# Optimization experiments

Hardware: AMD Instinct MI355X
Metric: run time of the kernel (lower is better)

Reference implementation:

```python
import jax, jax.numpy as jnp
import numpy as np

B = 256      # graphs per batch
N = 512      # nodes per graph
FEAT = 64    # num_features
H = 64       # nhid
DEG = 16     # avg degree
RATIO = 0.5  # pooling_ratio
E = B * N * DEG


def setup_inputs() -> dict:
    key = jax.random.key(0)
    ks = jax.random.split(key, 12)
    # edges constructed within each graph via offsets
    src_loc = jax.random.randint(ks[0], (B, N * DEG), 0, N)
    dst_loc = jax.random.randint(ks[1], (B, N * DEG), 0, N)
    offs = (jnp.arange(B) * N)[:, None]
    edge_src = (src_loc + offs).reshape(-1).astype(jnp.int32)
    edge_dst = (dst_loc + offs).reshape(-1).astype(jnp.int32)
    batch = jnp.repeat(jnp.arange(B, dtype=jnp.int32), N)
    x = jax.random.normal(ks[2], (B * N, FEAT), dtype=jnp.float32)
    edge_attr = jax.random.uniform(ks[3], (E,), dtype=jnp.float32) + 0.1
    s1 = 1.0 / np.sqrt(FEAT)
    s2 = 1.0 / np.sqrt(H)
    return {
        "x": x,
        "edge_attr": edge_attr,
        "W1": jax.random.normal(ks[4], (FEAT, H), jnp.float32) * s1,
        "b1": jnp.zeros((H,), jnp.float32),
        "Wp1": jax.random.normal(ks[5], (H, 1), jnp.float32) * s2,
        "bp1": jnp.zeros((1,), jnp.float32),
        "W2": jax.random.normal(ks[6], (H, H), jnp.float32) * s2,
        "b2": jnp.zeros((H,), jnp.float32),
        "Wp2": jax.random.normal(ks[7], (H, 1), jnp.float32) * s2,
        "bp2": jnp.zeros((1,), jnp.float32),
        "edge_src": edge_src,
        "edge_dst": edge_dst,
        "batch": batch,
    }


def gcn_conv(x, W, b, src, dst, ew, n):
    """PyG GCNConv: sym-normalized weighted adjacency + self-loops (weight 1)."""
    h = x @ W                                   # [n, out]
    deg = jnp.zeros((n,), x.dtype).at[dst].add(ew) + 1.0  # self-loop adds 1
    dinv = jax.lax.rsqrt(deg)
    coef = dinv[dst] * ew * dinv[src]           # [E]
    out = jnp.zeros_like(h).at[dst].add(coef[:, None] * h[src])
    out = out + h * (1.0 / deg)[:, None]        # self-loop term: deg^-0.5 * 1 * deg^-0.5
    return out + b


def sag_pool(x, src, dst, ew, Wp, bp, n_per):
    """SAGPool: score = GCNConv(x)->1, per-graph top-k, gate by tanh(score),
    filter edges (dropped edges represented by zero weight)."""
    n = x.shape[0]
    score = gcn_conv(x, Wp, bp, src, dst, ew, n)[:, 0]   # [n]
    k = int(np.ceil(RATIO * n_per))
    _, idx = jax.lax.top_k(score.reshape(B, n_per), k)   # [B, k] local indices
    perm = (idx + (jnp.arange(B) * n_per)[:, None]).reshape(-1)
    xn = x[perm] * jnp.tanh(score[perm])[:, None]        # [B*k, H]
    newid = jnp.full((n,), -1, jnp.int32).at[perm].set(
        jnp.arange(B * k, dtype=jnp.int32))
    ns, nd = newid[src], newid[dst]
    valid = (ns >= 0) & (nd >= 0)
    ew2 = jnp.where(valid, ew, 0.0)
    ns = jnp.where(valid, ns, 0)
    nd = jnp.where(valid, nd, 0)
    return xn, ns, nd, ew2, k


def readout(x, k):
    """[gmp || gap] per graph; each graph has exactly k nodes, contiguous."""
    xg = x.reshape(B, k, -1)
    return jnp.concatenate([xg.max(axis=1), xg.mean(axis=1)], axis=1)  # [B, 2H]


def reference(x, edge_attr, W1, b1, Wp1, bp1, W2, b2, Wp2, bp2,
              edge_src, edge_dst, batch):
    n0 = x.shape[0]
    h = jax.nn.relu(gcn_conv(x, W1, b1, edge_src, edge_dst, edge_attr, n0))
    h, s1, d1, w1e, k1 = sag_pool(h, edge_src, edge_dst, edge_attr, Wp1, bp1, N)
    x1 = readout(h, k1)
    h = jax.nn.relu(gcn_conv(h, W2, b2, s1, d1, w1e, B * k1))
    h, _, _, _, k2 = sag_pool(h, s1, d1, w1e, Wp2, bp2, k1)
    x2 = readout(h, k2)
    return (x1 + x2) / 2.0
```

## Files before the change

### kernel.cpp

```cpp
#include <hip/hip_runtime.h>
#include <math.h>

#define BG   256
#define NN   512
#define EPG  (NN * 16)
#define NE   (BG * EPG)
#define N0   (BG * NN)
#define K1   256
#define N1_  (BG * K1)
#define K2   128

__device__ __forceinline__ float4 f4fma(float s, float4 a, float4 c) {
    c.x = fmaf(s, a.x, c.x); c.y = fmaf(s, a.y, c.y);
    c.z = fmaf(s, a.z, c.z); c.w = fmaf(s, a.w, c.w);
    return c;
}

__device__ __forceinline__ void gemm_tile(const float* __restrict__ shx,
                                          const float4* __restrict__ W4,
                                          int row0, int rg, int cg, float4 a[4]) {
    float4 acc0 = make_float4(0.f, 0.f, 0.f, 0.f);
    float4 acc1 = acc0, acc2 = acc0, acc3 = acc0;
#pragma unroll
    for (int k4 = 0; k4 < 16; ++k4) {
        float4 xv0 = *(const float4*)&shx[(row0 + rg * 4 + 0) * 68 + k4 * 4];
        float4 xv1 = *(const float4*)&shx[(row0 + rg * 4 + 1) * 68 + k4 * 4];
        float4 xv2 = *(const float4*)&shx[(row0 + rg * 4 + 2) * 68 + k4 * 4];
        float4 xv3 = *(const float4*)&shx[(row0 + rg * 4 + 3) * 68 + k4 * 4];
        float4 wv0 = W4[(k4 * 4 + 0) * 16 + cg];
        float4 wv1 = W4[(k4 * 4 + 1) * 16 + cg];
        float4 wv2 = W4[(k4 * 4 + 2) * 16 + cg];
        float4 wv3 = W4[(k4 * 4 + 3) * 16 + cg];
        acc0 = f4fma(xv0.x, wv0, acc0); acc0 = f4fma(xv0.y, wv1, acc0);
        acc0 = f4fma(xv0.z, wv2, acc0); acc0 = f4fma(xv0.w, wv3, acc0);
        acc1 = f4fma(xv1.x, wv0, acc1); acc1 = f4fma(xv1.y, wv1, acc1);
        acc1 = f4fma(xv1.z, wv2, acc1); acc1 = f4fma(xv1.w, wv3, acc1);
        acc2 = f4fma(xv2.x, wv0, acc2); acc2 = f4fma(xv2.y, wv1, acc2);
        acc2 = f4fma(xv2.z, wv2, acc2); acc2 = f4fma(xv2.w, wv3, acc2);
        acc3 = f4fma(xv3.x, wv0, acc3); acc3 = f4fma(xv3.y, wv1, acc3);
        acc3 = f4fma(xv3.z, wv2, acc3); acc3 = f4fma(xv3.w, wv3, acc3);
    }
    a[0] = acc0; a[1] = acc1; a[2] = acc2; a[3] = acc3;
}

template <int NPG, int K, bool REMAP, bool FINAL>
__global__ __launch_bounds__(1024)
void stage_kernel(const int* __restrict__ esrc, const int* __restrict__ edst,
                  const float* __restrict__ eatt, const int* __restrict__ nid_in,
                  int* __restrict__ nid_out, int2* __restrict__ pairs,
                  const float4* __restrict__ X4, const float4* __restrict__ W4,
                  const float4* __restrict__ b4, const float4* __restrict__ wp4,
                  const float* __restrict__ bp,
                  float4* __restrict__ xn4, float* __restrict__ xr,
                  const float* __restrict__ x1r, float* __restrict__ out) {
    constexpr int PASSES = NPG / 32;
    constexpr int LPN = 1024 / NPG;
    constexpr int LOG_LPN = (LPN == 2) ? 1 : 2;
    constexpr int QF = 16 / LPN;
    constexpr int RLOG = (NPG == 512) ? 9 : 8;
    constexpr int RCH = NPG * NPG / 1024;
    constexpr int SH_A = NPG * 68;
    constexpr int TILES = NPG / 64, TPP = TILES / 2, TB = TPP / 2 ? TPP / 2 : 1;
    __shared__ __align__(16) float smem[SH_A + 4096 + 2 * NPG];
    float* shx = smem;
    float* S   = smem + SH_A;
    int*   cnt   = (int*)S;
    int*   rstl  = (int*)S + NPG;
    float* sdinv = S + 2 * NPG;
    int*   perm  = (int*)S + 3 * NPG;
    float* shp   = S + 4 * NPG;
    int*   scn   = (int*)S + 4 * NPG;
    float* wsum  = S + 5 * NPG;
    float* sbw   = S + 6 * NPG;
    int*   hist  = (int*)S + 6 * NPG + 64;
    int*   wtot  = (int*)S + 6 * NPG + 128;
    float4* smx  = (float4*)S;
    float4* ssm  = (float4*)(S + 2048);
    float* ssc   = S + 4096;
    int*   rnk   = (int*)S + 4096 + NPG;

    int g = blockIdx.x, nbase = g * NPG, e0 = g * EPG;
    int t = threadIdx.x;
    int lane16 = t & 15, lane = t & 63;

    int ed[16], es[16]; float ea[16];
    int xs = 0, xval = 0;
    float4 accA[TB][4], accB[TB][4];
    int tl = t - 512, q2 = (t & 511) >> 8, tq = t & 255;
    int rgg = tq >> 4, cgg = tq & 15;

    if (t < 512) {
        for (int i = t; i < NPG; i += 512) { cnt[i] = 0; wsum[i] = 0.f; }
        const int4*   edst4 = (const int4*)(edst + e0);
        const int4*   esrc4 = (const int4*)(esrc + e0);
        const float4* eatt4 = (const float4*)(eatt + e0);
#pragma unroll
        for (int c = 0; c < 4; ++c) {
            int ch = t + c * 512;
            int4   dd = edst4[ch];
            int4   ss = esrc4[ch];
            float4 ww = eatt4[ch];
            ed[c * 4 + 0] = dd.x; ed[c * 4 + 1] = dd.y; ed[c * 4 + 2] = dd.z; ed[c * 4 + 3] = dd.w;
            es[c * 4 + 0] = ss.x; es[c * 4 + 1] = ss.y; es[c * 4 + 2] = ss.z; es[c * 4 + 3] = ss.w;
            ea[c * 4 + 0] = ww.x; ea[c * 4 + 1] = ww.y; ea[c * 4 + 2] = ww.z; ea[c * 4 + 3] = ww.w;
        }
        if (REMAP) {
#pragma unroll
            for (int j = 0; j < 16; ++j) { ed[j] = nid_in[ed[j]]; es[j] = nid_in[es[j]]; }
        }
    } else {
        for (int i = tl; i < NPG * 16; i += 512) {
            int r = i >> 4, c4 = i & 15;
            *(float4*)&shx[r * 68 + c4 * 4] = X4[(size_t)nbase * 16 + i];
        }
        if (tl < 64) { sbw[tl] = ((const float*)b4)[tl]; hist[tl] = 0; }
        for (int i = tl; i < NPG; i += 512) rnk[i] = 0;
    }
    __syncthreads();
    if (t < 512) {
#pragma unroll
        for (int j = 0; j < 16; ++j) {
            bool valid = !REMAP || (ed[j] >= 0 && es[j] >= 0);
            if (valid) {
                int dl = ed[j] - nbase;
                atomicAdd(&cnt[dl], 1);
                atomicAdd(&wsum[dl], ea[j]);
            }
        }
    } else {
#pragma unroll
        for (int b = 0; b < TB; ++b)
            gemm_tile(shx, W4, (q2 * TPP + b) * 64, rgg, cgg, accA[b]);
    }
    __syncthreads();
    if (t < 512) {
        int wvid = t >> 6;
        xval = (t < NPG) ? cnt[t] : 0;
        xs = xval;
#pragma unroll
        for (int off = 1; off < 64; off <<= 1) {
            int v = __shfl_up(xs, off, 64);
            if (lane >= off) xs += v;
        }
        if (lane == 63) wtot[wvid] = xs;
    } else {
#pragma unroll
        for (int b = 0; b < TB; ++b) {
            int row0 = (q2 * TPP + b) * 64;
            *(float4*)&shx[(row0 + rgg * 4 + 0) * 68 + cgg * 4] = accA[b][0];
            *(float4*)&shx[(row0 + rgg * 4 + 1) * 68 + cgg * 4] = accA[b][1];
            *(float4*)&shx[(row0 + rgg * 4 + 2) * 68 + cgg * 4] = accA[b][2];
            *(float4*)&shx[(row0 + rgg * 4 + 3) * 68 + cgg * 4] = accA[b][3];
        }
    }
    __syncthreads();
    if (t < 512) {
        int wvid = t >> 6;
        int woff = 0;
#pragma unroll
        for (int w = 0; w < 8; ++w) { int wt = wtot[w]; if (w < wvid) woff += wt; }
        xs += woff;
        if (t < NPG) {
            int st = xs - xval;
            rstl[t] = st;
            sdinv[t] = rsqrtf(wsum[t] + 1.0f);
            scn[t] = st;
        }
    } else {
#pragma unroll
        for (int b = 0; b < TB; ++b)
            gemm_tile(shx, W4, (q2 * TPP + TB + b) * 64, rgg, cgg, accB[b]);
    }
    __syncthreads();
    if (t < 512) {
#pragma unroll
        for (int j = 0; j < 16; ++j) {
            bool valid = !REMAP || (ed[j] >= 0 && es[j] >= 0);
            if (valid) {
                int dl = ed[j] - nbase, sl = es[j] - nbase;
                float cf = sdinv[dl] * ea[j] * sdinv[sl];
                int slot = atomicAdd(&scn[dl], 1);
                pairs[e0 + slot] = make_int2(sl, __float_as_int(cf));
            }
        }
    } else {
#pragma unroll
        for (int b = 0; b < TB; ++b) {
            int row0 = (q2 * TPP + TB + b) * 64;
            *(float4*)&shx[(row0 + rgg * 4 + 0) * 68 + cgg * 4] = accB[b][0];
            *(float4*)&shx[(row0 + rgg * 4 + 1) * 68 + cgg * 4] = accB[b][1];
            *(float4*)&shx[(row0 + rgg * 4 + 2) * 68 + cgg * 4] = accB[b][2];
            *(float4*)&shx[(row0 + rgg * 4 + 3) * 68 + cgg * 4] = accB[b][3];
        }
    }
    __syncthreads();

    for (int i = t; i < NPG; i += 1024) {
        int c = min(cnt[i], 63);
        atomicAdd(&hist[c], 1);
    }
    __syncthreads();
    if (t < 64) {
        int v = hist[t], s = v;
#pragma unroll
        for (int off = 1; off < 64; off <<= 1) {
            int u = __shfl_up(s, off, 64);
            if (lane >= off) s += u;
        }
        hist[t] = s - v;
    }
    __syncthreads();
    for (int i = t; i < NPG; i += 1024) {
        int c = min(cnt[i], 63);
        int pos = atomicAdd(&hist[c], 1);
        perm[pos] = i;
    }
    __syncthreads();
    {
        int idx2 = t >> LOG_LPN;
        int half = t & (LPN - 1);
        int nl = perm[idx2];
        int st = rstl[nl], cn = cnt[nl];
        float di = sdinv[nl], dii = di * di;
        const int2* pb = pairs + e0 + st;
        int fb = half * QF;
        float4 acc[QF];
#pragma unroll
        for (int c = 0; c < QF; ++c) {
            float4 xv = *(const float4*)&shx[nl * 68 + (fb + c) * 4];
            acc[c].x = fmaf(xv.x, dii, sbw[(fb + c) * 4 + 0]);
            acc[c].y = fmaf(xv.y, dii, sbw[(fb + c) * 4 + 1]);
            acc[c].z = fmaf(xv.z, dii, sbw[(fb + c) * 4 + 2]);
            acc[c].w = fmaf(xv.w, dii, sbw[(fb + c) * 4 + 3]);
        }
        int2 p0 = (cn > 0) ? pb[0] : make_int2(0, 0);
        int2 p1 = (cn > 1) ? pb[1] : make_int2(0, 0);
        for (int j = 0; j < cn; ++j) {
            int2 p2 = (j + 2 < cn) ? pb[j + 2] : make_int2(0, 0);
            float cfv = __int_as_float(p0.y);
            int   s   = p0.x;
#pragma unroll
            for (int c = 0; c < QF; ++c)
                acc[c] = f4fma(cfv, *(const float4*)&shx[s * 68 + (fb + c) * 4], acc[c]);
            p0 = p1; p1 = p2;
        }
#pragma unroll
        for (int c = 0; c < QF; ++c) {
            acc[c].x = fmaxf(acc[c].x, 0.f); acc[c].y = fmaxf(acc[c].y, 0.f);
            acc[c].z = fmaxf(acc[c].z, 0.f); acc[c].w = fmaxf(acc[c].w, 0.f);
        }
        __syncthreads();
#pragma unroll
        for (int c = 0; c < QF; ++c)
            *(float4*)&shx[nl * 68 + (fb + c) * 4] = acc[c];
    }
    __syncthreads();
    if (t < 512) {
        int wv8 = t >> 6, sub4 = (t >> 4) & 3;
        float4 w4 = wp4[lane16];
#pragma unroll
        for (int p = 0; p < PASSES; ++p) {
            int n2 = p * 32 + wv8 * 4 + sub4;
            float4 a = *(const float4*)&shx[n2 * 68 + lane16 * 4];
            float tt = a.x * w4.x + a.y * w4.y + a.z * w4.z + a.w * w4.w;
            tt += __shfl_xor(tt, 1, 64); tt += __shfl_xor(tt, 2, 64);
            tt += __shfl_xor(tt, 4, 64); tt += __shfl_xor(tt, 8, 64);
            if (lane16 == 0) shp[n2] = tt;
        }
    }
    __syncthreads();
    if (t < NPG) {
        int i = perm[t];
        int st = rstl[i], cn = cnt[i];
        float di = sdinv[i];
        const int2* pb = pairs + e0 + st;
        float a = fmaf(shp[i], di * di, bp[0]);
        int2 q0 = (cn > 0) ? pb[0] : make_int2(0, 0);
        int2 q1 = (cn > 1) ? pb[1] : make_int2(0, 0);
        for (int j = 0; j < cn; ++j) {
            int2 q2v = (j + 2 < cn) ? pb[j + 2] : make_int2(0, 0);
            a = fmaf(__int_as_float(q0.y), shp[q0.x], a);
            q0 = q1; q1 = q2v;
        }
        ssc[i] = a;
    }
    __syncthreads();
    {
        int part = t >> RLOG;
        int i = t & (NPG - 1);
        float si = ssc[i];
        int j0 = part * RCH;
        int rank = 0;
        for (int j = j0; j < j0 + RCH; j += 4) {
            float4 sj = *(const float4*)&ssc[j];
            rank += (sj.x > si) || (sj.x == si && j     < i);
            rank += (sj.y > si) || (sj.y == si && j + 1 < i);
            rank += (sj.z > si) || (sj.z == si && j + 2 < i);
            rank += (sj.w > si) || (sj.w == si && j + 3 < i);
        }
        atomicAdd(&rnk[i], rank);
    }
    __syncthreads();
    if (!FINAL)
        for (int i = t; i < NPG; i += 1024)
            nid_out[nbase + i] = (rnk[i] < K) ? (g * K + rnk[i]) : -1;
    float4 mx = make_float4(-3.402823466e38f, -3.402823466e38f, -3.402823466e38f, -3.402823466e38f);
    float4 sm = make_float4(0.f, 0.f, 0.f, 0.f);
    if (t < 512) {
        int wv8 = t >> 6, sub4 = (t >> 4) & 3;
#pragma unroll
        for (int p = 0; p < PASSES; ++p) {
            int n2 = p * 32 + wv8 * 4 + sub4;
            int r = rnk[n2];
            if (r < K) {
                float gt = tanhf(ssc[n2]);
                float4 v = *(const float4*)&shx[n2 * 68 + lane16 * 4];
                v.x *= gt; v.y *= gt; v.z *= gt; v.w *= gt;
                if (!FINAL) xn4[((size_t)g * K + r) * 16 + lane16] = v;
                mx.x = fmaxf(mx.x, v.x); mx.y = fmaxf(mx.y, v.y);
                mx.z = fmaxf(mx.z, v.z); mx.w = fmaxf(mx.w, v.w);
                sm.x += v.x; sm.y += v.y; sm.z += v.z; sm.w += v.w;
            }
        }
    }
    int grp = t >> 4;
    __syncthreads();
    if (t < 512) {
        smx[grp * 16 + lane16] = mx;
        ssm[grp * 16 + lane16] = sm;
    }
    __syncthreads();
    if (grp == 0) {
#pragma unroll
        for (int u = 1; u < 32; ++u) {
            float4 a = smx[u * 16 + lane16], b = ssm[u * 16 + lane16];
            mx.x = fmaxf(mx.x, a.x); mx.y = fmaxf(mx.y, a.y);
            mx.z = fmaxf(mx.z, a.z); mx.w = fmaxf(mx.w, a.w);
            sm.x += b.x; sm.y += b.y; sm.z += b.z; sm.w += b.w;
        }
        float invK = 1.f / K;
        int c = lane16 * 4;
        float mr[4] = {mx.x, mx.y, mx.z, mx.w};
        float ar[4] = {sm.x * invK, sm.y * invK, sm.z * invK, sm.w * invK};
#pragma unroll
        for (int u = 0; u < 4; ++u) {
            if (FINAL) {
                out[g * 128 + c + u]      = 0.5f * (x1r[g * 128 + c + u]      + mr[u]);
                out[g * 128 + 64 + c + u] = 0.5f * (x1r[g * 128 + 64 + c + u] + ar[u]);
            } else {
                xr[g * 128 + c + u]      = mr[u];
                xr[g * 128 + 64 + c + u] = ar[u];
            }
        }
    }
}

extern "C" void kernel_launch(void* const* d_in, const int* in_sizes, int n_in,
                              void* d_out, int out_size, void* d_ws, size_t ws_size,
                              hipStream_t stream) {
    const float* x    = (const float*)d_in[0];
    const float* eatt = (const float*)d_in[1];
    const float* W1   = (const float*)d_in[2];
    const float* b1   = (const float*)d_in[3];
    const float* Wp1  = (const float*)d_in[4];
    const float* bp1  = (const float*)d_in[5];
    const float* W2   = (const float*)d_in[6];
    const float* b2   = (const float*)d_in[7];
    const float* Wp2  = (const float*)d_in[8];
    const float* bp2  = (const float*)d_in[9];
    const int*   esrc = (const int*)d_in[10];
    const int*   edst = (const int*)d_in[11];
    float* out = (float*)d_out;

    float* ws = (float*)d_ws;
    size_t o = 0;
    float* A    = ws + o; o += (size_t)N0 * 64;
    float* xn1  = ws + o; o += (size_t)N1_ * 64;
    int2*  prs  = (int2*)(ws + o); o += (size_t)NE * 2;
    int*   rst  = (int*)(ws + o); o += N0;
    int*   rcn  = (int*)(ws + o); o += N0;
    float* dinv = ws + o; o += N0;
    int*   nid  = (int*)(ws + o); o += N0;
    float* x1r  = ws + o; o += BG * 128;
    (void)A; (void)rst; (void)rcn; (void)dinv;

    stage_kernel<NN, K1, false, false><<<BG, 1024, 0, stream>>>(
        esrc, edst, eatt, nullptr, nid, prs,
        (const float4*)x, (const float4*)W1, (const float4*)b1,
        (const float4*)Wp1, bp1, (float4*)xn1, x1r, nullptr, nullptr);
    stage_kernel<K1, K2, true, true><<<BG, 1024, 0, stream>>>(
        esrc, edst, eatt, nid, nullptr, prs,
        (const float4*)xn1, (const float4*)W2, (const float4*)b2,
        (const float4*)Wp2, bp2, nullptr, nullptr, x1r, out);
}
```

Measured before the change: 257.3 us.

## Fuse both GCN+SAGPool stages into one per-graph kernel kept in shared memory

Merges the two stage launches into one kernel per graph. The pooled features, the node remap and the first-readout vector now stay in shared memory instead of round-tripping through global memory. CSR pair writes are staged through LDS in two halves so the global stores are coalesced, and all 1024 threads now do edge preprocessing instead of splitting work with the GEMM. The cost is that the GEMM no longer overlaps the edge phase, and there are more barriers and larger shared-memory use per block.

```diff
diff --git a/kernel.cpp b/kernel.cpp
--- a/kernel.cpp
+++ b/kernel.cpp
@@ -5,10 +5,6 @@
 #define NN   512
 #define EPG  (NN * 16)
 #define NE   (BG * EPG)
-#define N0   (BG * NN)
-#define K1   256
-#define N1_  (BG * K1)
-#define K2   128
 
 __device__ __forceinline__ float4 f4fma(float s, float4 a, float4 c) {
     c.x = fmaf(s, a.x, c.x); c.y = fmaf(s, a.y, c.y);
@@ -43,162 +39,128 @@
     a[0] = acc0; a[1] = acc1; a[2] = acc2; a[3] = acc3;
 }
 
-template <int NPG, int K, bool REMAP, bool FINAL>
 __global__ __launch_bounds__(1024)
-void stage_kernel(const int* __restrict__ esrc, const int* __restrict__ edst,
-                  const float* __restrict__ eatt, const int* __restrict__ nid_in,
-                  int* __restrict__ nid_out, int2* __restrict__ pairs,
-                  const float4* __restrict__ X4, const float4* __restrict__ W4,
-                  const float4* __restrict__ b4, const float4* __restrict__ wp4,
-                  const float* __restrict__ bp,
-                  float4* __restrict__ xn4, float* __restrict__ xr,
-                  const float* __restrict__ x1r, float* __restrict__ out) {
-    constexpr int PASSES = NPG / 32;
-    constexpr int LPN = 1024 / NPG;
-    constexpr int LOG_LPN = (LPN == 2) ? 1 : 2;
-    constexpr int QF = 16 / LPN;
-    constexpr int RLOG = (NPG == 512) ? 9 : 8;
-    constexpr int RCH = NPG * NPG / 1024;
-    constexpr int SH_A = NPG * 68;
-    constexpr int TILES = NPG / 64, TPP = TILES / 2, TB = TPP / 2 ? TPP / 2 : 1;
-    __shared__ __align__(16) float smem[SH_A + 4096 + 2 * NPG];
-    float* shx = smem;
-    float* S   = smem + SH_A;
+void mega_kernel(const int* __restrict__ esrc, const int* __restrict__ edst,
+                 const float* __restrict__ eatt, int2* __restrict__ pairs,
+                 const float4* __restrict__ X4,
+                 const float4* __restrict__ W1_4, const float4* __restrict__ b1_4,
+                 const float4* __restrict__ wp1_4, const float* __restrict__ bp1,
+                 const float4* __restrict__ W2_4, const float4* __restrict__ b2_4,
+                 const float4* __restrict__ wp2_4, const float* __restrict__ bp2,
+                 float* __restrict__ out) {
+    __shared__ __align__(16) float smem[40720];
+    float* shx  = smem;
+    float* S    = smem + 34816;
     int*   cnt   = (int*)S;
-    int*   rstl  = (int*)S + NPG;
-    float* sdinv = S + 2 * NPG;
-    int*   perm  = (int*)S + 3 * NPG;
-    float* shp   = S + 4 * NPG;
-    int*   scn   = (int*)S + 4 * NPG;
-    float* wsum  = S + 5 * NPG;
-    float* sbw   = S + 6 * NPG;
-    int*   hist  = (int*)S + 6 * NPG + 64;
-    int*   wtot  = (int*)S + 6 * NPG + 128;
-    float4* smx  = (float4*)S;
-    float4* ssm  = (float4*)(S + 2048);
-    float* ssc   = S + 4096;
-    int*   rnk   = (int*)S + 4096 + NPG;
-
-    int g = blockIdx.x, nbase = g * NPG, e0 = g * EPG;
+    int*   rstl  = (int*)S + 512;
+    float* sdinv = S + 1024;
+    int*   perm  = (int*)S + 1536;
+    int*   scn   = (int*)S + 2048;
+    float* shp   = S + 2048;
+    float* wsum  = S + 2560;
+    float* ssc   = S + 2560;
+    int*   rnk   = (int*)S + 3072;
+    float* sbw   = S + 3584;
+    int*   hist  = (int*)S + 3648;
+    int*   wtot  = (int*)S + 3712;
+    float* x1rs  = S + 3728;
+    float4* redx = (float4*)(S + 3856);
+
+    int g = blockIdx.x, nb1 = g * NN, e0 = g * EPG;
     int t = threadIdx.x;
     int lane16 = t & 15, lane = t & 63;
 
-    int ed[16], es[16]; float ea[16];
-    int xs = 0, xval = 0;
-    float4 accA[TB][4], accB[TB][4];
-    int tl = t - 512, q2 = (t & 511) >> 8, tq = t & 255;
-    int rgg = tq >> 4, cgg = tq & 15;
-
-    if (t < 512) {
-        for (int i = t; i < NPG; i += 512) { cnt[i] = 0; wsum[i] = 0.f; }
+    for (int i = t; i < NN; i += 1024) { cnt[i] = 0; wsum[i] = 0.f; }
+    __syncthreads();
+    {
         const int4*   edst4 = (const int4*)(edst + e0);
         const int4*   esrc4 = (const int4*)(esrc + e0);
         const float4* eatt4 = (const float4*)(eatt + e0);
-#pragma unroll
-        for (int c = 0; c < 4; ++c) {
-            int ch = t + c * 512;
-            int4   dd = edst4[ch];
-            int4   ss = esrc4[ch];
-            float4 ww = eatt4[ch];
-            ed[c * 4 + 0] = dd.x; ed[c * 4 + 1] = dd.y; ed[c * 4 + 2] = dd.z; ed[c * 4 + 3] = dd.w;
-            es[c * 4 + 0] = ss.x; es[c * 4 + 1] = ss.y; es[c * 4 + 2] = ss.z; es[c * 4 + 3] = ss.w;
-            ea[c * 4 + 0] = ww.x; ea[c * 4 + 1] = ww.y; ea[c * 4 + 2] = ww.z; ea[c * 4 + 3] = ww.w;
-        }
-        if (REMAP) {
-#pragma unroll
-            for (int j = 0; j < 16; ++j) { ed[j] = nid_in[ed[j]]; es[j] = nid_in[es[j]]; }
-        }
-    } else {
-        for (int i = tl; i < NPG * 16; i += 512) {
-            int r = i >> 4, c4 = i & 15;
-            *(float4*)&shx[r * 68 + c4 * 4] = X4[(size_t)nbase * 16 + i];
-        }
-        if (tl < 64) { sbw[tl] = ((const float*)b4)[tl]; hist[tl] = 0; }
-        for (int i = tl; i < NPG; i += 512) rnk[i] = 0;
-    }
-    __syncthreads();
-    if (t < 512) {
-#pragma unroll
-        for (int j = 0; j < 16; ++j) {
-            bool valid = !REMAP || (ed[j] >= 0 && es[j] >= 0);
-            if (valid) {
-                int dl = ed[j] - nbase;
-                atomicAdd(&cnt[dl], 1);
-                atomicAdd(&wsum[dl], ea[j]);
-            }
-        }
-    } else {
-#pragma unroll
-        for (int b = 0; b < TB; ++b)
-            gemm_tile(shx, W4, (q2 * TPP + b) * 64, rgg, cgg, accA[b]);
-    }
-    __syncthreads();
-    if (t < 512) {
-        int wvid = t >> 6;
-        xval = (t < NPG) ? cnt[t] : 0;
-        xs = xval;
+        int ed[8], es[8]; float ea[8];
+#pragma unroll
+        for (int c = 0; c < 2; ++c) {
+            int ch = t + c * 1024;
+            int4 dd = edst4[ch]; int4 ss = esrc4[ch]; float4 ww = eatt4[ch];
+            ed[c*4+0]=dd.x; ed[c*4+1]=dd.y; ed[c*4+2]=dd.z; ed[c*4+3]=dd.w;
+            es[c*4+0]=ss.x; es[c*4+1]=ss.y; es[c*4+2]=ss.z; es[c*4+3]=ss.w;
+            ea[c*4+0]=ww.x; ea[c*4+1]=ww.y; ea[c*4+2]=ww.z; ea[c*4+3]=ww.w;
+        }
+#pragma unroll
+        for (int j = 0; j < 8; ++j) {
+            int dl = ed[j] - nb1;
+            atomicAdd(&cnt[dl], 1);
+            atomicAdd(&wsum[dl], ea[j]);
+        }
+        __syncthreads();
+        int wv = t >> 6;
+        int xval = (t < NN) ? cnt[t] : 0;
+        int xs = xval;
 #pragma unroll
         for (int off = 1; off < 64; off <<= 1) {
             int v = __shfl_up(xs, off, 64);
             if (lane >= off) xs += v;
         }
-        if (lane == 63) wtot[wvid] = xs;
-    } else {
-#pragma unroll
-        for (int b = 0; b < TB; ++b) {
-            int row0 = (q2 * TPP + b) * 64;
-            *(float4*)&shx[(row0 + rgg * 4 + 0) * 68 + cgg * 4] = accA[b][0];
-            *(float4*)&shx[(row0 + rgg * 4 + 1) * 68 + cgg * 4] = accA[b][1];
-            *(float4*)&shx[(row0 + rgg * 4 + 2) * 68 + cgg * 4] = accA[b][2];
-            *(float4*)&shx[(row0 + rgg * 4 + 3) * 68 + cgg * 4] = accA[b][3];
-        }
-    }
-    __syncthreads();
-    if (t < 512) {
-        int wvid = t >> 6;
+        if (lane == 63) wtot[wv] = xs;
+        __syncthreads();
         int woff = 0;
 #pragma unroll
-        for (int w = 0; w < 8; ++w) { int wt = wtot[w]; if (w < wvid) woff += wt; }
+        for (int w = 0; w < 16; ++w) { int wt = wtot[w]; if (w < wv) woff += wt; }
         xs += woff;
-        if (t < NPG) {
+        if (t < NN) {
             int st = xs - xval;
             rstl[t] = st;
             sdinv[t] = rsqrtf(wsum[t] + 1.0f);
             scn[t] = st;
         }
-    } else {
-#pragma unroll
-        for (int b = 0; b < TB; ++b)
-            gemm_tile(shx, W4, (q2 * TPP + TB + b) * 64, rgg, cgg, accB[b]);
-    }
-    __syncthreads();
-    if (t < 512) {
-#pragma unroll
-        for (int j = 0; j < 16; ++j) {
-            bool valid = !REMAP || (ed[j] >= 0 && es[j] >= 0);
-            if (valid) {
-                int dl = ed[j] - nbase, sl = es[j] - nbase;
-                float cf = sdinv[dl] * ea[j] * sdinv[sl];
-                int slot = atomicAdd(&scn[dl], 1);
-                pairs[e0 + slot] = make_int2(sl, __float_as_int(cf));
-            }
-        }
-    } else {
-#pragma unroll
-        for (int b = 0; b < TB; ++b) {
-            int row0 = (q2 * TPP + TB + b) * 64;
-            *(float4*)&shx[(row0 + rgg * 4 + 0) * 68 + cgg * 4] = accB[b][0];
-            *(float4*)&shx[(row0 + rgg * 4 + 1) * 68 + cgg * 4] = accB[b][1];
-            *(float4*)&shx[(row0 + rgg * 4 + 2) * 68 + cgg * 4] = accB[b][2];
-            *(float4*)&shx[(row0 + rgg * 4 + 3) * 68 + cgg * 4] = accB[b][3];
-        }
-    }
-    __syncthreads();
-
-    for (int i = t; i < NPG; i += 1024) {
-        int c = min(cnt[i], 63);
-        atomicAdd(&hist[c], 1);
-    }
+        __syncthreads();
+        int slots[8]; float cf[8];
+#pragma unroll
+        for (int j = 0; j < 8; ++j) {
+            int dl = ed[j] - nb1, sl = es[j] - nb1;
+            cf[j] = sdinv[dl] * ea[j] * sdinv[sl];
+            slots[j] = atomicAdd(&scn[dl], 1);
+        }
+        int2* lp = (int2*)smem;
+#pragma unroll
+        for (int j = 0; j < 8; ++j)
+            if (slots[j] < 4096)
+                lp[slots[j]] = make_int2(es[j] - nb1, __float_as_int(cf[j]));
+        __syncthreads();
+        for (int k = t; k < 4096; k += 1024) pairs[e0 + k] = lp[k];
+        __syncthreads();
+#pragma unroll
+        for (int j = 0; j < 8; ++j)
+            if (slots[j] >= 4096)
+                lp[slots[j] - 4096] = make_int2(es[j] - nb1, __float_as_int(cf[j]));
+        __syncthreads();
+        for (int k = t; k < 4096; k += 1024) pairs[e0 + 4096 + k] = lp[k];
+        __syncthreads();
+    }
+    for (int i = t; i < NN * 16; i += 1024) {
+        int r = i >> 4, c4 = i & 15;
+        *(float4*)&shx[r * 68 + c4 * 4] = X4[(size_t)nb1 * 16 + i];
+    }
+    if (t < 64) { sbw[t] = ((const float*)b1_4)[t]; hist[t] = 0; }
+    for (int i = t; i < NN; i += 1024) rnk[i] = 0;
+    __syncthreads();
+    {
+        int q = t >> 8, tq = t & 255, rg = tq >> 4, cg = tq & 15;
+        float4 ac[2][4];
+#pragma unroll
+        for (int tt = 0; tt < 2; ++tt)
+            gemm_tile(shx, W1_4, (tt * 4 + q) * 64, rg, cg, ac[tt]);
+        __syncthreads();
+#pragma unroll
+        for (int tt = 0; tt < 2; ++tt) {
+            int row0 = (tt * 4 + q) * 64;
+            *(float4*)&shx[(row0 + rg * 4 + 0) * 68 + cg * 4] = ac[tt][0];
+            *(float4*)&shx[(row0 + rg * 4 + 1) * 68 + cg * 4] = ac[tt][1];
+            *(float4*)&shx[(row0 + rg * 4 + 2) * 68 + cg * 4] = ac[tt][2];
+            *(float4*)&shx[(row0 + rg * 4 + 3) * 68 + cg * 4] = ac[tt][3];
+        }
+    }
+    __syncthreads();
+    for (int i = t; i < NN; i += 1024) atomicAdd(&hist[min(cnt[i], 63)], 1);
     __syncthreads();
     if (t < 64) {
         int v = hist[t], s = v;
@@ -210,23 +172,20 @@
         hist[t] = s - v;
     }
     __syncthreads();
-    for (int i = t; i < NPG; i += 1024) {
-        int c = min(cnt[i], 63);
-        int pos = atomicAdd(&hist[c], 1);
+    for (int i = t; i < NN; i += 1024) {
+        int pos = atomicAdd(&hist[min(cnt[i], 63)], 1);
         perm[pos] = i;
     }
     __syncthreads();
     {
-        int idx2 = t >> LOG_LPN;
-        int half = t & (LPN - 1);
+        int idx2 = t >> 1, half = t & 1, fb = half * 8;
         int nl = perm[idx2];
         int st = rstl[nl], cn = cnt[nl];
         float di = sdinv[nl], dii = di * di;
         const int2* pb = pairs + e0 + st;
-        int fb = half * QF;
-        float4 acc[QF];
-#pragma unroll
-        for (int c = 0; c < QF; ++c) {
+        float4 acc[8];
+#pragma unroll
+        for (int c = 0; c < 8; ++c) {
             float4 xv = *(const float4*)&shx[nl * 68 + (fb + c) * 4];
             acc[c].x = fmaf(xv.x, dii, sbw[(fb + c) * 4 + 0]);
             acc[c].y = fmaf(xv.y, dii, sbw[(fb + c) * 4 + 1]);
@@ -240,26 +199,26 @@
             float cfv = __int_as_float(p0.y);
             int   s   = p0.x;
 #pragma unroll
-            for (int c = 0; c < QF; ++c)
+            for (int c = 0; c < 8; ++c)
                 acc[c] = f4fma(cfv, *(const float4*)&shx[s * 68 + (fb + c) * 4], acc[c]);
             p0 = p1; p1 = p2;
         }
 #pragma unroll
-        for (int c = 0; c < QF; ++c) {
+        for (int c = 0; c < 8; ++c) {
             acc[c].x = fmaxf(acc[c].x, 0.f); acc[c].y = fmaxf(acc[c].y, 0.f);
             acc[c].z = fmaxf(acc[c].z, 0.f); acc[c].w = fmaxf(acc[c].w, 0.f);
         }
         __syncthreads();
 #pragma unroll
-        for (int c = 0; c < QF; ++c)
+        for (int c = 0; c < 8; ++c)
             *(float4*)&shx[nl * 68 + (fb + c) * 4] = acc[c];
     }
     __syncthreads();
     if (t < 512) {
         int wv8 = t >> 6, sub4 = (t >> 4) & 3;
-        float4 w4 = wp4[lane16];
-#pragma unroll
-        for (int p = 0; p < PASSES; ++p) {
+        float4 w4 = wp1_4[lane16];
+#pragma unroll
+        for (int p = 0; p < 16; ++p) {
             int n2 = p * 32 + wv8 * 4 + sub4;
             float4 a = *(const float4*)&shx[n2 * 68 + lane16 * 4];
             float tt = a.x * w4.x + a.y * w4.y + a.z * w4.z + a.w * w4.w;
@@ -269,12 +228,12 @@
         }
     }
     __syncthreads();
-    if (t < NPG) {
+    if (t < NN) {
         int i = perm[t];
         int st = rstl[i], cn = cnt[i];
         float di = sdinv[i];
         const int2* pb = pairs + e0 + st;
-        float a = fmaf(shp[i], di * di, bp[0]);
+        float a = fmaf(shp[i], di * di, bp1[0]);
         int2 q0 = (cn > 0) ? pb[0] : make_int2(0, 0);
         int2 q1 = (cn > 1) ? pb[1] : make_int2(0, 0);
         for (int j = 0; j < cn; ++j) {
@@ -286,12 +245,10 @@
     }
     __syncthreads();
     {
-        int part = t >> RLOG;
-        int i = t & (NPG - 1);
+        int part = t >> 9, i = t & 511;
         float si = ssc[i];
-        int j0 = part * RCH;
-        int rank = 0;
-        for (int j = j0; j < j0 + RCH; j += 4) {
+        int j0 = part * 256, rank = 0;
+        for (int j = j0; j < j0 + 256; j += 4) {
             float4 sj = *(const float4*)&ssc[j];
             rank += (sj.x > si) || (sj.x == si && j     < i);
             rank += (sj.y > si) || (sj.y == si && j + 1 < i);
@@ -301,55 +258,312 @@
         atomicAdd(&rnk[i], rank);
     }
     __syncthreads();
-    if (!FINAL)
-        for (int i = t; i < NPG; i += 1024)
-            nid_out[nbase + i] = (rnk[i] < K) ? (g * K + rnk[i]) : -1;
-    float4 mx = make_float4(-3.402823466e38f, -3.402823466e38f, -3.402823466e38f, -3.402823466e38f);
-    float4 sm = make_float4(0.f, 0.f, 0.f, 0.f);
+    {
+        float4 mx = make_float4(-3.402823466e38f, -3.402823466e38f, -3.402823466e38f, -3.402823466e38f);
+        float4 sm = make_float4(0.f, 0.f, 0.f, 0.f);
+        if (t < 512) {
+            int wv8 = t >> 6, sub4 = (t >> 4) & 3;
+#pragma unroll
+            for (int p = 0; p < 16; ++p) {
+                int n2 = p * 32 + wv8 * 4 + sub4;
+                int r = rnk[n2];
+                if (r < 256) {
+                    float gt = tanhf(ssc[n2]);
+                    float4 v = *(const float4*)&shx[n2 * 68 + lane16 * 4];
+                    v.x *= gt; v.y *= gt; v.z *= gt; v.w *= gt;
+                    mx.x = fmaxf(mx.x, v.x); mx.y = fmaxf(mx.y, v.y);
+                    mx.z = fmaxf(mx.z, v.z); mx.w = fmaxf(mx.w, v.w);
+                    sm.x += v.x; sm.y += v.y; sm.z += v.z; sm.w += v.w;
+                }
+            }
+        }
+        int grp = t >> 4;
+        __syncthreads();
+        if (t < 512) redx[grp * 16 + lane16] = mx;
+        __syncthreads();
+        float mr[4] = {0, 0, 0, 0};
+        if (grp == 0) {
+#pragma unroll
+            for (int u = 1; u < 32; ++u) {
+                float4 a = redx[u * 16 + lane16];
+                mx.x = fmaxf(mx.x, a.x); mx.y = fmaxf(mx.y, a.y);
+                mx.z = fmaxf(mx.z, a.z); mx.w = fmaxf(mx.w, a.w);
+            }
+            mr[0] = mx.x; mr[1] = mx.y; mr[2] = mx.z; mr[3] = mx.w;
+        }
+        __syncthreads();
+        if (t < 512) redx[grp * 16 + lane16] = sm;
+        __syncthreads();
+        if (grp == 0) {
+#pragma unroll
+            for (int u = 1; u < 32; ++u) {
+                float4 b = redx[u * 16 + lane16];
+                sm.x += b.x; sm.y += b.y; sm.z += b.z; sm.w += b.w;
+            }
+            float invK = 1.f / 256.f;
+            int c = lane16 * 4;
+            float ar[4] = {sm.x * invK, sm.y * invK, sm.z * invK, sm.w * invK};
+#pragma unroll
+            for (int u = 0; u < 4; ++u) {
+                x1rs[c + u]      = mr[u];
+                x1rs[64 + c + u] = ar[u];
+            }
+        }
+    }
+    {
+        int* nor = perm;
+        __syncthreads();
+        for (int i = t; i < NN; i += 1024) {
+            int r = rnk[i];
+            if (r < 256) nor[r] = i;
+        }
+        __syncthreads();
+        float4 stash[4];
+        int rr[4], cc[4];
+#pragma unroll
+        for (int u = 0; u < 4; ++u) {
+            int idx = t + u * 1024;
+            rr[u] = idx >> 4; cc[u] = idx & 15;
+            int n = nor[rr[u]];
+            float gt = tanhf(ssc[n]);
+            float4 v = *(const float4*)&shx[n * 68 + cc[u] * 4];
+            v.x *= gt; v.y *= gt; v.z *= gt; v.w *= gt;
+            stash[u] = v;
+        }
+        __syncthreads();
+#pragma unroll
+        for (int u = 0; u < 4; ++u)
+            *(float4*)&shx[rr[u] * 68 + cc[u] * 4] = stash[u];
+        __syncthreads();
+    }
+
+    int2* lp2 = (int2*)&shx[256 * 68];
+    for (int i = t; i < 256; i += 1024) { cnt[i] = 0; wsum[i] = 0.f; }
+    __syncthreads();
+    {
+        const int4*   edst4 = (const int4*)(edst + e0);
+        const int4*   esrc4 = (const int4*)(esrc + e0);
+        const float4* eatt4 = (const float4*)(eatt + e0);
+        int ed[8], es[8]; float ea[8];
+#pragma unroll
+        for (int c = 0; c < 2; ++c) {
+            int ch = t + c * 1024;
+            int4 dd = edst4[ch]; int4 ss = esrc4[ch]; float4 ww = eatt4[ch];
+            ed[c*4+0]=dd.x; ed[c*4+1]=dd.y; ed[c*4+2]=dd.z; ed[c*4+3]=dd.w;
+            es[c*4+0]=ss.x; es[c*4+1]=ss.y; es[c*4+2]=ss.z; es[c*4+3]=ss.w;
+            ea[c*4+0]=ww.x; ea[c*4+1]=ww.y; ea[c*4+2]=ww.z; ea[c*4+3]=ww.w;
+        }
+#pragma unroll
+        for (int j = 0; j < 8; ++j) {
+            int rd = rnk[ed[j] - nb1], rs = rnk[es[j] - nb1];
+            ed[j] = (rd < 256) ? rd : -1;
+            es[j] = (rs < 256) ? rs : -1;
+        }
+#pragma unroll
+        for (int j = 0; j < 8; ++j) {
+            if (ed[j] >= 0 && es[j] >= 0) {
+                atomicAdd(&cnt[ed[j]], 1);
+                atomicAdd(&wsum[ed[j]], ea[j]);
+            }
+        }
+        __syncthreads();
+        int wv = t >> 6;
+        int xval = (t < 256) ? cnt[t] : 0;
+        int xs = xval;
+#pragma unroll
+        for (int off = 1; off < 64; off <<= 1) {
+            int v = __shfl_up(xs, off, 64);
+            if (lane >= off) xs += v;
+        }
+        if (lane == 63) wtot[wv] = xs;
+        __syncthreads();
+        int woff = 0;
+#pragma unroll
+        for (int w = 0; w < 16; ++w) { int wt = wtot[w]; if (w < wv) woff += wt; }
+        xs += woff;
+        if (t < 256) {
+            int st = xs - xval;
+            rstl[t] = st;
+            sdinv[t] = rsqrtf(wsum[t] + 1.0f);
+            scn[t] = st;
+        }
+        __syncthreads();
+        int slots[8]; float cf[8];
+#pragma unroll
+        for (int j = 0; j < 8; ++j) {
+            slots[j] = -1;
+            if (ed[j] >= 0 && es[j] >= 0) {
+                cf[j] = sdinv[ed[j]] * ea[j] * sdinv[es[j]];
+                slots[j] = atomicAdd(&scn[ed[j]], 1);
+            }
+        }
+#pragma unroll
+        for (int j = 0; j < 8; ++j)
+            if (slots[j] >= 0)
+                lp2[slots[j]] = make_int2(es[j], __float_as_int(cf[j]));
+        for (int i = t; i < 256; i += 1024) rnk[i] = 0;
+        if (t < 64) { sbw[t] = ((const float*)b2_4)[t]; hist[t] = 0; }
+        __syncthreads();
+    }
+    {
+        int q = t >> 8, tq = t & 255, rg = tq >> 4, cg = tq & 15;
+        float4 a4[4];
+        gemm_tile(shx, W2_4, q * 64, rg, cg, a4);
+        __syncthreads();
+        int row0 = q * 64;
+        *(float4*)&shx[(row0 + rg * 4 + 0) * 68 + cg * 4] = a4[0];
+        *(float4*)&shx[(row0 + rg * 4 + 1) * 68 + cg * 4] = a4[1];
+        *(float4*)&shx[(row0 + rg * 4 + 2) * 68 + cg * 4] = a4[2];
+        *(float4*)&shx[(row0 + rg * 4 + 3) * 68 + cg * 4] = a4[3];
+    }
+    __syncthreads();
+    for (int i = t; i < 256; i += 1024) atomicAdd(&hist[min(cnt[i], 63)], 1);
+    __syncthreads();
+    if (t < 64) {
+        int v = hist[t], s = v;
+#pragma unroll
+        for (int off = 1; off < 64; off <<= 1) {
+            int u = __shfl_up(s, off, 64);
+            if (lane >= off) s += u;
+        }
+        hist[t] = s - v;
+    }
+    __syncthreads();
+    for (int i = t; i < 256; i += 1024) {
+        int pos = atomicAdd(&hist[min(cnt[i], 63)], 1);
+        perm[pos] = i;
+    }
+    __syncthreads();
+    {
+        int idx2 = t >> 2, half = t & 3, fb = half * 4;
+        int nl = perm[idx2];
+        int st = rstl[nl], cn = cnt[nl];
+        float di = sdinv[nl], dii = di * di;
+        const int2* pb = lp2 + st;
+        float4 acc[4];
+#pragma unroll
+        for (int c = 0; c < 4; ++c) {
+            float4 xv = *(const float4*)&shx[nl * 68 + (fb + c) * 4];
+            acc[c].x = fmaf(xv.x, dii, sbw[(fb + c) * 4 + 0]);
+            acc[c].y = fmaf(xv.y, dii, sbw[(fb + c) * 4 + 1]);
+            acc[c].z = fmaf(xv.z, dii, sbw[(fb + c) * 4 + 2]);
+            acc[c].w = fmaf(xv.w, dii, sbw[(fb + c) * 4 + 3]);
+        }
+        int2 p0 = (cn > 0) ? pb[0] : make_int2(0, 0);
+        int2 p1 = (cn > 1) ? pb[1] : make_int2(0, 0);
+        for (int j = 0; j < cn; ++j) {
+            int2 p2 = (j + 2 < cn) ? pb[j + 2] : make_int2(0, 0);
+            float cfv = __int_as_float(p0.y);
+            int   s   = p0.x;
+#pragma unroll
+            for (int c = 0; c < 4; ++c)
+                acc[c] = f4fma(cfv, *(const float4*)&shx[s * 68 + (fb + c) * 4], acc[c]);
+            p0 = p1; p1 = p2;
+        }
+#pragma unroll
+        for (int c = 0; c < 4; ++c) {
+            acc[c].x = fmaxf(acc[c].x, 0.f); acc[c].y = fmaxf(acc[c].y, 0.f);
+            acc[c].z = fmaxf(acc[c].z, 0.f); acc[c].w = fmaxf(acc[c].w, 0.f);
+        }
+        __syncthreads();
+#pragma unroll
+        for (int c = 0; c < 4; ++c)
+            *(float4*)&shx[nl * 68 + (fb + c) * 4] = acc[c];
+    }
+    __syncthreads();
     if (t < 512) {
         int wv8 = t >> 6, sub4 = (t >> 4) & 3;
-#pragma unroll
-        for (int p = 0; p < PASSES; ++p) {
+        float4 w4 = wp2_4[lane16];
+#pragma unroll
+        for (int p = 0; p < 8; ++p) {
             int n2 = p * 32 + wv8 * 4 + sub4;
-            int r = rnk[n2];
-            if (r < K) {
-                float gt = tanhf(ssc[n2]);
-                float4 v = *(const float4*)&shx[n2 * 68 + lane16 * 4];
-                v.x *= gt; v.y *= gt; v.z *= gt; v.w *= gt;
-                if (!FINAL) xn4[((size_t)g * K + r) * 16 + lane16] = v;
-                mx.x = fmaxf(mx.x, v.x); mx.y = fmaxf(mx.y, v.y);
-                mx.z = fmaxf(mx.z, v.z); mx.w = fmaxf(mx.w, v.w);
-                sm.x += v.x; sm.y += v.y; sm.z += v.z; sm.w += v.w;
-            }
-        }
-    }
-    int grp = t >> 4;
-    __syncthreads();
-    if (t < 512) {
-        smx[grp * 16 + lane16] = mx;
-        ssm[grp * 16 + lane16] = sm;
-    }
-    __syncthreads();
-    if (grp == 0) {
-#pragma unroll
-        for (int u = 1; u < 32; ++u) {
-            float4 a = smx[u * 16 + lane16], b = ssm[u * 16 + lane16];
-            mx.x = fmaxf(mx.x, a.x); mx.y = fmaxf(mx.y, a.y);
-            mx.z = fmaxf(mx.z, a.z); mx.w = fmaxf(mx.w, a.w);
-            sm.x += b.x; sm.y += b.y; sm.z += b.z; sm.w += b.w;
-        }
-        float invK = 1.f / K;
-        int c = lane16 * 4;
-        float mr[4] = {mx.x, mx.y, mx.z, mx.w};
-        float ar[4] = {sm.x * invK, sm.y * invK, sm.z * invK, sm.w * invK};
-#pragma unroll
-        for (int u = 0; u < 4; ++u) {
-            if (FINAL) {
-                out[g * 128 + c + u]      = 0.5f * (x1r[g * 128 + c + u]      + mr[u]);
-                out[g * 128 + 64 + c + u] = 0.5f * (x1r[g * 128 + 64 + c + u] + ar[u]);
-            } else {
-                xr[g * 128 + c + u]      = mr[u];
-                xr[g * 128 + 64 + c + u] = ar[u];
+            float4 a = *(const float4*)&shx[n2 * 68 + lane16 * 4];
+            float tt = a.x * w4.x + a.y * w4.y + a.z * w4.z + a.w * w4.w;
+            tt += __shfl_xor(tt, 1, 64); tt += __shfl_xor(tt, 2, 64);
+            tt += __shfl_xor(tt, 4, 64); tt += __shfl_xor(tt, 8, 64);
+            if (lane16 == 0) shp[n2] = tt;
+        }
+    }
+    __syncthreads();
+    if (t < 256) {
+        int i = perm[t];
+        int st = rstl[i], cn = cnt[i];
+        float di = sdinv[i];
+        const int2* pb = lp2 + st;
+        float a = fmaf(shp[i], di * di, bp2[0]);
+        int2 q0 = (cn > 0) ? pb[0] : make_int2(0, 0);
+        int2 q1 = (cn > 1) ? pb[1] : make_int2(0, 0);
+        for (int j = 0; j < cn; ++j) {
+            int2 q2v = (j + 2 < cn) ? pb[j + 2] : make_int2(0, 0);
+            a = fmaf(__int_as_float(q0.y), shp[q0.x], a);
+            q0 = q1; q1 = q2v;
+        }
+        ssc[i] = a;
+    }
+    __syncthreads();
+    {
+        int part = t >> 8, i = t & 255;
+        float si = ssc[i];
+        int j0 = part * 64, rank = 0;
+        for (int j = j0; j < j0 + 64; j += 4) {
+            float4 sj = *(const float4*)&ssc[j];
+            rank += (sj.x > si) || (sj.x == si && j     < i);
+            rank += (sj.y > si) || (sj.y == si && j + 1 < i);
+            rank += (sj.z > si) || (sj.z == si && j + 2 < i);
+            rank += (sj.w > si) || (sj.w == si && j + 3 < i);
+        }
+        atomicAdd(&rnk[i], rank);
+    }
+    __syncthreads();
+    {
+        float4 mx = make_float4(-3.402823466e38f, -3.402823466e38f, -3.402823466e38f, -3.402823466e38f);
+        float4 sm = make_float4(0.f, 0.f, 0.f, 0.f);
+        if (t < 512) {
+            int wv8 = t >> 6, sub4 = (t >> 4) & 3;
+#pragma unroll
+            for (int p = 0; p < 8; ++p) {
+                int n2 = p * 32 + wv8 * 4 + sub4;
+                int r = rnk[n2];
+                if (r < 128) {
+                    float gt = tanhf(ssc[n2]);
+                    float4 v = *(const float4*)&shx[n2 * 68 + lane16 * 4];
+                    v.x *= gt; v.y *= gt; v.z *= gt; v.w *= gt;
+                    mx.x = fmaxf(mx.x, v.x); mx.y = fmaxf(mx.y, v.y);
+                    mx.z = fmaxf(mx.z, v.z); mx.w = fmaxf(mx.w, v.w);
+                    sm.x += v.x; sm.y += v.y; sm.z += v.z; sm.w += v.w;
+                }
+            }
+        }
+        int grp = t >> 4;
+        __syncthreads();
+        if (t < 512) redx[grp * 16 + lane16] = mx;
+        __syncthreads();
+        float mr[4] = {0, 0, 0, 0};
+        if (grp == 0) {
+#pragma unroll
+            for (int u = 1; u < 32; ++u) {
+                float4 a = redx[u * 16 + lane16];
+                mx.x = fmaxf(mx.x, a.x); mx.y = fmaxf(mx.y, a.y);
+                mx.z = fmaxf(mx.z, a.z); mx.w = fmaxf(mx.w, a.w);
+            }
+            mr[0] = mx.x; mr[1] = mx.y; mr[2] = mx.z; mr[3] = mx.w;
+        }
+        __syncthreads();
+        if (t < 512) redx[grp * 16 + lane16] = sm;
+        __syncthreads();
+        if (grp == 0) {
+#pragma unroll
+            for (int u = 1; u < 32; ++u) {
+                float4 b = redx[u * 16 + lane16];
+                sm.x += b.x; sm.y += b.y; sm.z += b.z; sm.w += b.w;
+            }
+            float invK = 1.f / 128.f;
+            int c = lane16 * 4;
+            float ar[4] = {sm.x * invK, sm.y * invK, sm.z * invK, sm.w * invK};
+#pragma unroll
+            for (int u = 0; u < 4; ++u) {
+                out[g * 128 + c + u]      = 0.5f * (x1rs[c + u]      + mr[u]);
+                out[g * 128 + 64 + c + u] = 0.5f * (x1rs[64 + c + u] + ar[u]);
             }
         }
     }
@@ -372,24 +586,11 @@
     const int*   edst = (const int*)d_in[11];
     float* out = (float*)d_out;
 
-    float* ws = (float*)d_ws;
-    size_t o = 0;
-    float* A    = ws + o; o += (size_t)N0 * 64;
-    float* xn1  = ws + o; o += (size_t)N1_ * 64;
-    int2*  prs  = (int2*)(ws + o); o += (size_t)NE * 2;
-    int*   rst  = (int*)(ws + o); o += N0;
-    int*   rcn  = (int*)(ws + o); o += N0;
-    float* dinv = ws + o; o += N0;
-    int*   nid  = (int*)(ws + o); o += N0;
-    float* x1r  = ws + o; o += BG * 128;
-    (void)A; (void)rst; (void)rcn; (void)dinv;
-
-    stage_kernel<NN, K1, false, false><<<BG, 1024, 0, stream>>>(
-        esrc, edst, eatt, nullptr, nid, prs,
-        (const float4*)x, (const float4*)W1, (const float4*)b1,
-        (const float4*)Wp1, bp1, (float4*)xn1, x1r, nullptr, nullptr);
-    stage_kernel<K1, K2, true, true><<<BG, 1024, 0, stream>>>(
-        esrc, edst, eatt, nid, nullptr, prs,
-        (const float4*)xn1, (const float4*)W2, (const float4*)b2,
-        (const float4*)Wp2, bp2, nullptr, nullptr, x1r, out);
+    int2* prs = (int2*)d_ws;
+
+    mega_kernel<<<BG, 1024, 0, stream>>>(
+        esrc, edst, eatt, prs, (const float4*)x,
+        (const float4*)W1, (const float4*)b1, (const float4*)Wp1, bp1,
+        (const float4*)W2, (const float4*)b2, (const float4*)Wp2, bp2,
+        out);
 }
```

Result: faster. 209.9 us (-18.4%).
